# Kernel tuning notes

Measured on AMD Instinct MI355X. Metric: run time of the kernel, lower is better.

Reference implementation:

```python
import jax, jax.numpy as jnp
import numpy as np

B, N, D, DS, LAT, FD, NF = 2, 384, 128, 3, 256, 1, 2
NPOS = DS * (2 * 5 + 1)  # 3 + 3*2*5 = 33
FREQS = np.linspace(1.0, 32.0, 5)  # torch.linspace(1, 2**5, 5)
EPS = 1e-5


def _bn(x, g, b):
    # BatchNorm1d, train-mode batch stats: normalize per channel over (batch, points)
    m = jnp.mean(x, axis=(0, 1))
    v = jnp.var(x, axis=(0, 1))
    return (x - m) * jax.lax.rsqrt(v + EPS) * g + b


def _tblock(xyz4, f, Wq, Wk, Wv, Wg1, bg1, Wg2, bg2, Wpe, bpe, g, b):
    # group_all=True full vector attention. f: [B,n,D], xyz4: [B,n,3]
    q = f @ Wq.T
    k = f @ Wk.T
    v = f @ Wv.T
    # knn_xyz gathered under no_grad in torch -> stop_gradient on the key side
    pd = xyz4[:, :, None] - jax.lax.stop_gradient(xyz4)[:, None]  # [B,n,n,3]
    parts = [pd]
    for fr in FREQS:
        parts.append(jnp.sin(pd * fr))
        parts.append(jnp.cos(pd * fr))
    pos = jnp.concatenate(parts, axis=-1) @ Wpe.T + bpe  # [B,n,n,D]
    edges = q[:, :, None] - k[:, None] + pos  # [B,n,n,D]
    h = jax.nn.relu(edges @ Wg1.T + bg1)
    attn = jax.nn.softmax(h @ Wg2.T + bg2, axis=-2)  # softmax over neighbor axis
    res = jnp.sum(attn * (v[:, None] + pos), axis=2)  # einsum bmnf,bmnf->bmf
    return _bn(res + f, g, b)


def setup_inputs() -> dict:
    key = jax.random.key(0)
    ks = iter(jax.random.split(key, 40))
    def rn(shape, s=0.05):
        return jax.random.normal(next(ks), shape, dtype=jnp.float32) * s
    z = lambda *s: jnp.zeros(s, jnp.float32)
    o = lambda *s: jnp.ones(s, jnp.float32)
    nb = NF + 1  # begin block + nfinal blocks
    return {
        "xyz": jax.random.normal(next(ks), (B, N, DS), dtype=jnp.float32),
        "feats": jax.random.normal(next(ks), (B, N, FD), dtype=jnp.float32),
        "enc_W": rn((D, FD)), "enc_b": z(D),
        "tb_Wq": rn((nb, D, D)), "tb_Wk": rn((nb, D, D)), "tb_Wv": rn((nb, D, D)),
        "tb_Wg1": rn((nb, D, D)), "tb_bg1": z(nb, D),
        "tb_Wg2": rn((nb, D, D)), "tb_bg2": z(nb, D),
        "tb_Wpe": rn((nb, D, NPOS)), "tb_bpe": z(nb, D),
        "tb_gamma": o(nb, D), "tb_beta": z(nb, D),
        "em_W1": rn((NF, D, D)), "em_b1": z(NF, D),
        "em_W2": rn((NF, D, D)), "em_b2": z(NF, D),
        "em_gamma": o(NF, D), "em_beta": z(NF, D),
        "fcf_W1": rn((LAT, D)), "fcf_b1": z(LAT),
        "fcf_W2": rn((LAT, LAT)), "fcf_b2": z(LAT),
    }


def reference(xyz, feats, enc_W, enc_b, tb_Wq, tb_Wk, tb_Wv, tb_Wg1, tb_bg1,
              tb_Wg2, tb_bg2, tb_Wpe, tb_bpe, tb_gamma, tb_beta,
              em_W1, em_b1, em_W2, em_b2, em_gamma, em_beta,
              fcf_W1, fcf_b1, fcf_W2, fcf_b2):
    f = feats @ enc_W.T + enc_b  # enc_feats
    x4 = xyz * 4.0
    for i in range(NF + 1):  # i=0: transformer_begin; i>=1: final transformers
        f = _tblock(x4, f, tb_Wq[i], tb_Wk[i], tb_Wv[i], tb_Wg1[i], tb_bg1[i],
                    tb_Wg2[i], tb_bg2[i], tb_Wpe[i], tb_bpe[i], tb_gamma[i], tb_beta[i])
        if i > 0:
            j = i - 1  # ElementwiseMLP: bn(x + relu(conv2(relu(conv1(x)))))
            y = jax.nn.relu(f @ em_W1[j].T + em_b1[j])
            y = jax.nn.relu(y @ em_W2[j].T + em_b2[j])
            f = _bn(f + y, em_gamma[j], em_beta[j])
    e = jax.nn.relu(f @ fcf_W1.T + fcf_b1) @ fcf_W2.T + fcf_b2
    return jnp.max(e, axis=1)  # lat_rep [B, lat_dim]
```

## Files before the change

kernel.cpp:

```cpp
#include <hip/hip_runtime.h>
#include <hip/hip_bf16.h>

#define B_ 2
#define N_ 384
#define D_ 128
#define LAT_ 256
#define NPOS_ 33
#define ROWS_ (B_*N_)
#define NT_ 64
#define ITERS_ (N_/NT_)

typedef __attribute__((ext_vector_type(8))) short bf16x8;
typedef __attribute__((ext_vector_type(4))) float f32x4;

#define MFMA(a,b,c) __builtin_amdgcn_mfma_f32_16x16x32_bf16((a),(b),(c),0,0,0)

__device__ __forceinline__ unsigned short f2bf(float x) {
    unsigned int u = __float_as_uint(x);
    u += 0x7FFFu + ((u >> 16) & 1u);
    return (unsigned short)(u >> 16);
}
__device__ __forceinline__ float bf2f(unsigned short u) {
    return __uint_as_float(((unsigned int)u) << 16);
}

__device__ __forceinline__ float bn_apply(float x, const float* stats, const float* gam,
                                          const float* bet, int d) {
    float s  = stats[d], sq = stats[128 + d];
    float mean = s * (1.f/ROWS_);
    float var  = sq * (1.f/ROWS_) - mean*mean;
    return (x - mean) * rsqrtf(var + 1e-5f) * gam[d] + bet[d];
}

__global__ __launch_bounds__(256) void fprep_kernel(const float* __restrict__ xyz,
                                                    unsigned short* __restrict__ gF) {
    int i = blockIdx.x*256 + threadIdx.x;
    if (i >= ROWS_*64) return;
    int n = i >> 6, q = i & 63;
    float val;
    if (q == 0) val = 1.f;
    else if (q < 4) val = 4.f*xyz[n*3 + (q-1)];
    else if (q < 34) {
        int u = q-4, fi = u/6, rem = u - fi*6, j = rem >> 1;
        const float fr = fi==0?1.f:(fi==1?8.75f:(fi==2?16.5f:(fi==3?24.25f:32.f)));
        float a = fr*4.f*xyz[n*3+j];
        val = (rem & 1) ? __sinf(a) : __cosf(a);
    } else val = 0.f;
    gF[n*64 + (q ^ ((n & 7) << 3))] = f2bf(val);
}

__global__ __launch_bounds__(128) void psi_kernel(
    const float* __restrict__ Wg1, const float* __restrict__ Wpe,
    const float* __restrict__ bpe, float* __restrict__ psi)
{
    const int blk = blockIdx.x, layer = blk / 34, p = blk - layer*34;
    const float* wg1 = Wg1 + layer*D_*D_;
    __shared__ float col[D_];
    const int e = threadIdx.x;
    col[e] = (p < NPOS_) ? Wpe[layer*D_*NPOS_ + e*NPOS_ + p] : bpe[layer*D_ + e];
    __syncthreads();
    float acc = 0.f;
    #pragma unroll 4
    for (int d4 = 0; d4 < 32; ++d4) {
        float4 w = *(const float4*)(wg1 + e*D_ + d4*4);
        acc += w.x*col[d4*4] + w.y*col[d4*4+1] + w.z*col[d4*4+2] + w.w*col[d4*4+3];
    }
    psi[layer*D_*34 + e*34 + p] = acc;
}

__global__ __launch_bounds__(256) void enc_kernel(const float* __restrict__ feats,
                           const float* __restrict__ W,
                           const float* __restrict__ bias,
                           float* __restrict__ f) {
    int i = blockIdx.x*256 + threadIdx.x;
    if (i >= ROWS_*D_) return;
    int r = i >> 7, d = i & 127;
    f[i] = feats[r]*W[d] + bias[d];
}

__global__ __launch_bounds__(128) void qkvkw_kernel(const float* __restrict__ graw,
    const float* __restrict__ stats, const float* __restrict__ gam, const float* __restrict__ bet,
    int use_stats,
    const float* __restrict__ Wq, const float* __restrict__ Wk, const float* __restrict__ Wv,
    const float* __restrict__ Wg1, const float* __restrict__ bg1,
    float* __restrict__ hb, unsigned short* __restrict__ kw16, unsigned short* __restrict__ v16)
{
    __shared__ float rows[4][D_], qrows[4][D_], krows[4][D_];
    const int r0 = blockIdx.x*4, d = threadIdx.x;
    #pragma unroll
    for (int rr = 0; rr < 4; ++rr) {
        float x = graw[(r0+rr)*D_ + d];
        if (use_stats) x = bn_apply(x, stats, gam, bet, d);
        rows[rr][d] = x;
    }
    __syncthreads();
    float aq[4] = {0,0,0,0}, ak[4] = {0,0,0,0}, av[4] = {0,0,0,0};
    #pragma unroll 4
    for (int e4 = 0; e4 < D_/4; ++e4) {
        float4 wq = *(const float4*)(Wq + d*D_ + e4*4);
        float4 wk = *(const float4*)(Wk + d*D_ + e4*4);
        float4 wv = *(const float4*)(Wv + d*D_ + e4*4);
        #pragma unroll
        for (int rr = 0; rr < 4; ++rr) {
            float4 x = *(const float4*)&rows[rr][e4*4];
            aq[rr] += wq.x*x.x + wq.y*x.y + wq.z*x.z + wq.w*x.w;
            ak[rr] += wk.x*x.x + wk.y*x.y + wk.z*x.z + wk.w*x.w;
            av[rr] += wv.x*x.x + wv.y*x.y + wv.z*x.z + wv.w*x.w;
        }
    }
    #pragma unroll
    for (int rr = 0; rr < 4; ++rr) {
        v16[(r0+rr)*D_ + d] = f2bf(av[rr]);
        qrows[rr][d] = aq[rr];
        krows[rr][d] = ak[rr];
    }
    __syncthreads();
    float hq[4], hk[4] = {0,0,0,0};
    #pragma unroll
    for (int rr = 0; rr < 4; ++rr) hq[rr] = bg1[d];
    #pragma unroll 4
    for (int e4 = 0; e4 < D_/4; ++e4) {
        float4 w = *(const float4*)(Wg1 + d*D_ + e4*4);
        #pragma unroll
        for (int rr = 0; rr < 4; ++rr) {
            float4 xq = *(const float4*)&qrows[rr][e4*4];
            float4 xk = *(const float4*)&krows[rr][e4*4];
            hq[rr] += w.x*xq.x + w.y*xq.y + w.z*xq.z + w.w*xq.w;
            hk[rr] += w.x*xk.x + w.y*xk.y + w.z*xk.z + w.w*xk.w;
        }
    }
    #pragma unroll
    for (int rr = 0; rr < 4; ++rr) {
        hb[(r0+rr)*D_ + d]   = hq[rr];
        kw16[(r0+rr)*D_ + d] = f2bf(hk[rr]);
    }
}

__global__ __launch_bounds__(512) void attn_mfma_kernel(
    const float* __restrict__ xyz, const float* __restrict__ graw,
    const float* __restrict__ stats_in, const float* __restrict__ gam_in,
    const float* __restrict__ bet_in, int use_stats,
    const float* __restrict__ hbb,
    const unsigned short* __restrict__ kwb, const unsigned short* __restrict__ vb,
    const unsigned short* __restrict__ gF,
    const float* __restrict__ psiL,
    const float* __restrict__ Wpe, const float* __restrict__ bpe,
    const float* __restrict__ Wg2, const float* __restrict__ bg2,
    float* __restrict__ gout, float* __restrict__ stats_out)
{
    __shared__ unsigned short sF[NT_*64];
    __shared__ unsigned short sH[NT_*128];
    __shared__ float sRed[4*128];

    const int t   = threadIdx.x;
    const int w   = t >> 6;
    const int l   = t & 63;
    const int lr  = l & 15;
    const int lg  = l >> 4;
    const int rb2 = w >> 2;
    const int ct0 = (w & 3) * 2;

    const int row  = blockIdx.x;
    const int b    = row / N_;
    const int brow = b * N_;

    uint4 freg = *(const uint4*)(gF + (size_t)brow*64 + t*8);
    unsigned short kw_us[2][2][4];
    unsigned short v_us[2][2][4];
    auto loadKW = [&](int n0) {
        #pragma unroll
        for (int rt = 0; rt < 2; ++rt)
        #pragma unroll
        for (int ct = 0; ct < 2; ++ct) {
            const int d = (ct0 + ct)*16 + lr;
            #pragma unroll
            for (int r = 0; r < 4; ++r) {
                const int rr = rb2*32 + rt*16 + lg*4 + r;
                kw_us[rt][ct][r] = kwb[(brow + n0 + rr)*D_ + d];
            }
        }
    };
    auto loadV = [&](int n0) {
        #pragma unroll
        for (int rt = 0; rt < 2; ++rt)
        #pragma unroll
        for (int ct = 0; ct < 2; ++ct) {
            const int d = (ct0 + ct)*16 + lr;
            #pragma unroll
            for (int r = 0; r < 4; ++r) {
                const int rr = rb2*32 + rt*16 + lg*4 + r;
                v_us[rt][ct][r] = vb[(brow + n0 + rr)*D_ + d];
            }
        }
    };
    loadKW(0);

    bf16x8 bWg2[2][4], bG[2][2], bT[2][2];
    float  hb_c[2], bg2_c[2];

    const float xm0 = 4.f*xyz[row*3+0];
    const float xm1 = 4.f*xyz[row*3+1];
    const float xm2 = 4.f*xyz[row*3+2];

    #pragma unroll
    for (int ct = 0; ct < 2; ++ct) {
        const int dout = (ct0 + ct) * 16 + lr;
        #pragma unroll
        for (int kt = 0; kt < 4; ++kt) {
            const float* p2 = Wg2 + dout * D_ + kt * 32 + lg * 8;
            float4 c0 = *(const float4*)(p2);
            float4 c1 = *(const float4*)(p2 + 4);
            bf16x8 v2;
            v2[0]=(short)f2bf(c0.x); v2[1]=(short)f2bf(c0.y); v2[2]=(short)f2bf(c0.z); v2[3]=(short)f2bf(c0.w);
            v2[4]=(short)f2bf(c1.x); v2[5]=(short)f2bf(c1.y); v2[6]=(short)f2bf(c1.z); v2[7]=(short)f2bf(c1.w);
            bWg2[ct][kt] = v2;
        }
        {
            const float* wrow = Wpe + dout*NPOS_;
            float bias = bpe[dout] + wrow[0]*xm0 + wrow[1]*xm1 + wrow[2]*xm2;
            #pragma unroll
            for (int kt = 0; kt < 2; ++kt) {
                bf16x8 g;
                #pragma unroll
                for (int e = 0; e < 8; ++e) {
                    const int qq = kt*32 + lg*8 + e;
                    float val;
                    if (qq == 0) val = bias;
                    else if (qq < 4) val = -wrow[qq-1];
                    else if (qq < 34) {
                        const int u = qq - 4, fi = u/6, rem = u - fi*6, j = rem >> 1;
                        const float Ws = wrow[3 + 6*fi + j];
                        const float Wc = wrow[3 + 6*fi + 3 + j];
                        const float fr = fi==0?1.f:(fi==1?8.75f:(fi==2?16.5f:(fi==3?24.25f:32.f)));
                        const float am = fr * (j==0?xm0:(j==1?xm1:xm2));
                        const float sm = __sinf(am), cm = __cosf(am);
                        val = (rem & 1) ? (Wc*sm - Ws*cm) : (Ws*sm + Wc*cm);
                    } else val = 0.f;
                    g[e] = (short)f2bf(val);
                }
                bG[ct][kt] = g;
            }
        }
        {
            const float* prow = psiL + dout*34;
            float bias = prow[33] + prow[0]*xm0 + prow[1]*xm1 + prow[2]*xm2;
            #pragma unroll
            for (int kt = 0; kt < 2; ++kt) {
                bf16x8 g;
                #pragma unroll
                for (int e = 0; e < 8; ++e) {
                    const int qq = kt*32 + lg*8 + e;
                    float val;
                    if (qq == 0) val = bias;
                    else if (qq < 4) val = -prow[qq-1];
                    else if (qq < 34) {
                        const int u = qq - 4, fi = u/6, rem = u - fi*6, j = rem >> 1;
                        const float Ws = prow[3 + 6*fi + j];
                        const float Wc = prow[3 + 6*fi + 3 + j];
                        const float fr = fi==0?1.f:(fi==1?8.75f:(fi==2?16.5f:(fi==3?24.25f:32.f)));
                        const float am = fr * (j==0?xm0:(j==1?xm1:xm2));
                        const float sm = __sinf(am), cm = __cosf(am);
                        val = (rem & 1) ? (Wc*sm - Ws*cm) : (Ws*sm + Wc*cm);
                    } else val = 0.f;
                    g[e] = (short)f2bf(val);
                }
                bT[ct][kt] = g;
            }
        }
        hb_c[ct]  = hbb[row*D_ + dout];
        bg2_c[ct] = bg2[dout];
    }

    *(uint4*)&sF[t*8] = freg;
    __syncthreads();

    float res_p[2] = {0.f, 0.f}, s_p[2] = {0.f, 0.f};
    f32x4 pos[2][2];

    for (int it = 0; it < ITERS_; ++it) {
        const int n0 = it * NT_;
        const bool more = (it < ITERS_ - 1);

        loadV(n0);
        if (more) freg = *(const uint4*)(gF + (size_t)(brow + n0 + NT_)*64 + t*8);
        f32x4 hacc[2][2];
        #pragma unroll
        for (int rt = 0; rt < 2; ++rt) {
            const int r16 = rb2*32 + rt*16 + lr;
            const int sw  = (r16 & 7) << 3;
            bf16x8 a0 = *(const bf16x8*)&sF[(r16*64 +  0 + lg*8) ^ sw];
            bf16x8 a1 = *(const bf16x8*)&sF[(r16*64 + 32 + lg*8) ^ sw];
            #pragma unroll
            for (int ct = 0; ct < 2; ++ct) {
                f32x4 z = {0.f,0.f,0.f,0.f};
                hacc[rt][ct] = MFMA(a1, bT[ct][1], MFMA(a0, bT[ct][0], z));
                pos[rt][ct]  = MFMA(a1, bG[ct][1], MFMA(a0, bG[ct][0], z));
            }
        }
        #pragma unroll
        for (int rt = 0; rt < 2; ++rt)
        #pragma unroll
        for (int ct = 0; ct < 2; ++ct) {
            const int d = (ct0 + ct)*16 + lr;
            #pragma unroll
            for (int r = 0; r < 4; ++r) {
                const int rr = rb2*32 + rt*16 + lg*4 + r;
                const float hv = hacc[rt][ct][r] + hb_c[ct] - bf2f(kw_us[rt][ct][r]);
                sH[(rr*128 + d) ^ ((rr & 7) << 3)] = f2bf(fmaxf(hv, 0.f));
            }
        }
        __syncthreads();

        if (more) {
            *(uint4*)&sF[t*8] = freg;
            loadKW(n0 + NT_);
        }
        f32x4 lacc[2][2];
        #pragma unroll
        for (int rt = 0; rt < 2; ++rt) {
            lacc[rt][0] = (f32x4){bg2_c[0], bg2_c[0], bg2_c[0], bg2_c[0]};
            lacc[rt][1] = (f32x4){bg2_c[1], bg2_c[1], bg2_c[1], bg2_c[1]};
            #pragma unroll
            for (int kt = 0; kt < 4; ++kt) {
                const int r16 = rb2*32 + rt*16 + lr;
                const int idx = (r16*128 + kt*32 + lg*8) ^ ((r16 & 7) << 3);
                bf16x8 a = *(const bf16x8*)&sH[idx];
                lacc[rt][0] = MFMA(a, bWg2[0][kt], lacc[rt][0]);
                lacc[rt][1] = MFMA(a, bWg2[1][kt], lacc[rt][1]);
            }
        }
        #pragma unroll
        for (int rt = 0; rt < 2; ++rt)
        #pragma unroll
        for (int ct = 0; ct < 2; ++ct) {
            #pragma unroll
            for (int r = 0; r < 4; ++r) {
                const float wgt = __expf(lacc[rt][ct][r]);
                const float vp  = bf2f(v_us[rt][ct][r]) + pos[rt][ct][r];
                res_p[ct] += wgt * vp;
                s_p[ct]   += wgt;
            }
        }
        __syncthreads();
    }

    #pragma unroll
    for (int ct = 0; ct < 2; ++ct) {
        #pragma unroll
        for (int off = 16; off < 64; off <<= 1) {
            res_p[ct] += __shfl_xor(res_p[ct], off, 64);
            s_p[ct]   += __shfl_xor(s_p[ct], off, 64);
        }
    }
    if (lg == 0) {
        #pragma unroll
        for (int ct = 0; ct < 2; ++ct) {
            const int d = (ct0 + ct)*16 + lr;
            sRed[(rb2*2+0)*128 + d] = res_p[ct];
            sRed[(rb2*2+1)*128 + d] = s_p[ct];
        }
    }
    __syncthreads();
    if (t < D_) {
        const float rsum = sRed[t]       + sRed[2*128 + t];
        const float ssum = sRed[128 + t] + sRed[3*128 + t];
        float fres = graw[row*D_ + t];
        if (use_stats) fres = bn_apply(fres, stats_in, gam_in, bet_in, t);
        const float val = rsum / ssum + fres;
        gout[row*D_ + t] = val;
        atomicAdd(&stats_out[t], val);
        atomicAdd(&stats_out[128 + t], val*val);
    }
}

__global__ __launch_bounds__(128) void em_kernel(const float* __restrict__ graw,
    const float* __restrict__ stats_in, const float* __restrict__ gam_in, const float* __restrict__ bet_in,
    const float* __restrict__ W1, const float* __restrict__ b1,
    const float* __restrict__ W2, const float* __restrict__ b2,
    float* __restrict__ gout, float* __restrict__ stats_out)
{
    __shared__ float rows[4][D_], y1[4][D_];
    const int r0 = blockIdx.x*4, d = threadIdx.x;
    float fn[4];
    #pragma unroll
    for (int rr = 0; rr < 4; ++rr) {
        fn[rr] = bn_apply(graw[(r0+rr)*D_ + d], stats_in, gam_in, bet_in, d);
        rows[rr][d] = fn[rr];
    }
    __syncthreads();
    float a[4] = {b1[d], b1[d], b1[d], b1[d]};
    #pragma unroll 4
    for (int e4 = 0; e4 < D_/4; ++e4) {
        float4 w = *(const float4*)(W1 + d*D_ + e4*4);
        #pragma unroll
        for (int rr = 0; rr < 4; ++rr) {
            float4 x = *(const float4*)&rows[rr][e4*4];
            a[rr] += w.x*x.x + w.y*x.y + w.z*x.z + w.w*x.w;
        }
    }
    #pragma unroll
    for (int rr = 0; rr < 4; ++rr) y1[rr][d] = fmaxf(a[rr], 0.f);
    __syncthreads();
    float a2[4] = {b2[d], b2[d], b2[d], b2[d]};
    #pragma unroll 4
    for (int e4 = 0; e4 < D_/4; ++e4) {
        float4 w = *(const float4*)(W2 + d*D_ + e4*4);
        #pragma unroll
        for (int rr = 0; rr < 4; ++rr) {
            float4 x = *(const float4*)&y1[rr][e4*4];
            a2[rr] += w.x*x.x + w.y*x.y + w.z*x.z + w.w*x.w;
        }
    }
    #pragma unroll
    for (int rr = 0; rr < 4; ++rr) {
        const float g2 = fn[rr] + fmaxf(a2[rr], 0.f);
        gout[(r0+rr)*D_ + d] = g2;
        atomicAdd(&stats_out[d], g2);
        atomicAdd(&stats_out[128+d], g2*g2);
    }
}

__global__ __launch_bounds__(256) void final_kernel(const float* __restrict__ graw,
    const float* __restrict__ stats_in, const float* __restrict__ gam_in, const float* __restrict__ bet_in,
    const float* __restrict__ W1, const float* __restrict__ b1,
    const float* __restrict__ W2, const float* __restrict__ b2,
    float* __restrict__ e_ws)
{
    __shared__ float rows[4][D_];
    __shared__ float h1[4][LAT_];
    const int r0 = blockIdx.x*4, t = threadIdx.x;
    for (int i = t; i < 4*D_; i += 256) {
        const int rr = i >> 7, d = i & 127;
        rows[rr][d] = bn_apply(graw[(r0+rr)*D_ + d], stats_in, gam_in, bet_in, d);
    }
    __syncthreads();
    float a[4] = {b1[t], b1[t], b1[t], b1[t]};
    #pragma unroll 4
    for (int e4 = 0; e4 < D_/4; ++e4) {
        float4 w = *(const float4*)(W1 + t*D_ + e4*4);
        #pragma unroll
        for (int rr = 0; rr < 4; ++rr) {
            float4 x = *(const float4*)&rows[rr][e4*4];
            a[rr] += w.x*x.x + w.y*x.y + w.z*x.z + w.w*x.w;
        }
    }
    #pragma unroll
    for (int rr = 0; rr < 4; ++rr) h1[rr][t] = fmaxf(a[rr], 0.f);
    __syncthreads();
    float a2[4] = {b2[t], b2[t], b2[t], b2[t]};
    #pragma unroll 4
    for (int e4 = 0; e4 < LAT_/4; ++e4) {
        float4 w = *(const float4*)(W2 + t*LAT_ + e4*4);
        #pragma unroll
        for (int rr = 0; rr < 4; ++rr) {
            float4 x = *(const float4*)&h1[rr][e4*4];
            a2[rr] += w.x*x.x + w.y*x.y + w.z*x.z + w.w*x.w;
        }
    }
    #pragma unroll
    for (int rr = 0; rr < 4; ++rr) e_ws[(r0+rr)*LAT_ + t] = a2[rr];
}

__global__ __launch_bounds__(256) void maxred_kernel(const float* __restrict__ e_ws,
                                                     float* __restrict__ out)
{
    int b = blockIdx.x, l = threadIdx.x;
    float m = -INFINITY;
    #pragma unroll 8
    for (int n=0;n<N_;n++) m = fmaxf(m, e_ws[(b*N_+n)*LAT_+l]);
    out[b*LAT_+l] = m;
}

extern "C" void kernel_launch(void* const* d_in, const int* in_sizes, int n_in,
                              void* d_out, int out_size, void* d_ws, size_t ws_size,
                              hipStream_t stream) {
    (void)in_sizes; (void)n_in; (void)out_size; (void)ws_size;
    const float* xyz    = (const float*)d_in[0];
    const float* feats  = (const float*)d_in[1];
    const float* enc_W  = (const float*)d_in[2];
    const float* enc_b  = (const float*)d_in[3];
    const float* tb_Wq  = (const float*)d_in[4];
    const float* tb_Wk  = (const float*)d_in[5];
    const float* tb_Wv  = (const float*)d_in[6];
    const float* tb_Wg1 = (const float*)d_in[7];
    const float* tb_bg1 = (const float*)d_in[8];
    const float* tb_Wg2 = (const float*)d_in[9];
    const float* tb_bg2 = (const float*)d_in[10];
    const float* tb_Wpe = (const float*)d_in[11];
    const float* tb_bpe = (const float*)d_in[12];
    const float* tb_gamma = (const float*)d_in[13];
    const float* tb_beta  = (const float*)d_in[14];
    const float* em_W1  = (const float*)d_in[15];
    const float* em_b1  = (const float*)d_in[16];
    const float* em_W2  = (const float*)d_in[17];
    const float* em_b2  = (const float*)d_in[18];
    const float* em_gamma = (const float*)d_in[19];
    const float* em_beta  = (const float*)d_in[20];
    const float* fcf_W1 = (const float*)d_in[21];
    const float* fcf_b1 = (const float*)d_in[22];
    const float* fcf_W2 = (const float*)d_in[23];
    const float* fcf_b2 = (const float*)d_in[24];
    float* out = (float*)d_out;

    float* ws   = (float*)d_ws;
    float* buf0 = ws;
    float* buf1 = buf0 + ROWS_*D_;
    float* hbb  = buf1 + ROWS_*D_;
    float* ebuf = hbb  + ROWS_*D_;
    float* psi  = ebuf + ROWS_*LAT_;
    float* stats = psi + 3*D_*34;
    float* sA0 = stats;
    float* sA1 = stats + 256;
    float* sE1 = stats + 512;
    float* sA2 = stats + 768;
    float* sE2 = stats + 1024;
    unsigned short* kwbuf = (unsigned short*)(stats + 5*256);
    unsigned short* vbuf  = kwbuf + ROWS_*D_;
    unsigned short* gF    = vbuf + ROWS_*D_;

    hipMemsetAsync(stats, 0, 5*256*sizeof(float), stream);

    fprep_kernel<<<(ROWS_*64+255)/256, 256, 0, stream>>>(xyz, gF);
    psi_kernel<<<3*34, 128, 0, stream>>>(tb_Wg1, tb_Wpe, tb_bpe, psi);
    enc_kernel<<<(ROWS_*D_+255)/256, 256, 0, stream>>>(feats, enc_W, enc_b, buf0);

    const float* gz = tb_gamma;
    qkvkw_kernel<<<ROWS_/4, 128, 0, stream>>>(buf0, gz, gz, gz, 0,
        tb_Wq, tb_Wk, tb_Wv, tb_Wg1, tb_bg1, hbb, kwbuf, vbuf);
    attn_mfma_kernel<<<ROWS_, 512, 0, stream>>>(xyz, buf0, gz, gz, gz, 0,
        hbb, kwbuf, vbuf, gF, psi,
        tb_Wpe, tb_bpe, tb_Wg2, tb_bg2, buf1, sA0);
    qkvkw_kernel<<<ROWS_/4, 128, 0, stream>>>(buf1, sA0, tb_gamma, tb_beta, 1,
        tb_Wq + 1*D_*D_, tb_Wk + 1*D_*D_, tb_Wv + 1*D_*D_,
        tb_Wg1 + 1*D_*D_, tb_bg1 + 1*D_, hbb, kwbuf, vbuf);
    attn_mfma_kernel<<<ROWS_, 512, 0, stream>>>(xyz, buf1, sA0, tb_gamma, tb_beta, 1,
        hbb, kwbuf, vbuf, gF, psi + 1*D_*34,
        tb_Wpe + 1*D_*NPOS_, tb_bpe + 1*D_, tb_Wg2 + 1*D_*D_, tb_bg2 + 1*D_, buf0, sA1);
    em_kernel<<<ROWS_/4, 128, 0, stream>>>(buf0, sA1, tb_gamma + 1*D_, tb_beta + 1*D_,
                                           em_W1, em_b1, em_W2, em_b2, buf1, sE1);
    qkvkw_kernel<<<ROWS_/4, 128, 0, stream>>>(buf1, sE1, em_gamma, em_beta, 1,
        tb_Wq + 2*D_*D_, tb_Wk + 2*D_*D_, tb_Wv + 2*D_*D_,
        tb_Wg1 + 2*D_*D_, tb_bg1 + 2*D_, hbb, kwbuf, vbuf);
    attn_mfma_kernel<<<ROWS_, 512, 0, stream>>>(xyz, buf1, sE1, em_gamma, em_beta, 1,
        hbb, kwbuf, vbuf, gF, psi + 2*D_*34,
        tb_Wpe + 2*D_*NPOS_, tb_bpe + 2*D_, tb_Wg2 + 2*D_*D_, tb_bg2 + 2*D_, buf0, sA2);
    em_kernel<<<ROWS_/4, 128, 0, stream>>>(buf0, sA2, tb_gamma + 2*D_, tb_beta + 2*D_,
                                           em_W1 + 1*D_*D_, em_b1 + 1*D_,
                                           em_W2 + 1*D_*D_, em_b2 + 1*D_, buf1, sE2);
    final_kernel<<<ROWS_/4, 256, 0, stream>>>(buf1, sE2, em_gamma + 1*D_, em_beta + 1*D_,
                                              fcf_W1, fcf_b1, fcf_W2, fcf_b2, ebuf);
    maxred_kernel<<<B_, 256, 0, stream>>>(ebuf, out);
}
```

Before: 556.9 us.

## Precompose Wg1 with Wq/Wk, merge prep kernels, shrink per-block row counts

Folds Wg1 into Wq and Wk by precomputing the products Wg1·Wq and Wg1·Wk once per call in a merged prep kernel, so the per-row QKV kernel needs one matvec stage instead of two. The fprep, psi and enc kernels are merged with this weight precomputation into a single launch to cut launch overhead. The em and final kernels process fewer rows per block (1 and 2) to spread work across more blocks. The cost is an extra 2x3 128x128 matrix-product precompute each call, less weight reuse per block, and a small change in rounding order.

```diff
diff --git a/kernel.cpp b/kernel.cpp
--- a/kernel.cpp
+++ b/kernel.cpp
@@ -32,108 +32,102 @@
     return (x - mean) * rsqrtf(var + 1e-5f) * gam[d] + bet[d];
 }
 
-__global__ __launch_bounds__(256) void fprep_kernel(const float* __restrict__ xyz,
-                                                    unsigned short* __restrict__ gF) {
-    int i = blockIdx.x*256 + threadIdx.x;
-    if (i >= ROWS_*64) return;
-    int n = i >> 6, q = i & 63;
-    float val;
-    if (q == 0) val = 1.f;
-    else if (q < 4) val = 4.f*xyz[n*3 + (q-1)];
-    else if (q < 34) {
-        int u = q-4, fi = u/6, rem = u - fi*6, j = rem >> 1;
-        const float fr = fi==0?1.f:(fi==1?8.75f:(fi==2?16.5f:(fi==3?24.25f:32.f)));
-        float a = fr*4.f*xyz[n*3+j];
-        val = (rem & 1) ? __sinf(a) : __cosf(a);
-    } else val = 0.f;
-    gF[n*64 + (q ^ ((n & 7) << 3))] = f2bf(val);
-}
-
-__global__ __launch_bounds__(128) void psi_kernel(
-    const float* __restrict__ Wg1, const float* __restrict__ Wpe,
-    const float* __restrict__ bpe, float* __restrict__ psi)
+#define PB_FPREP 192
+#define PB_PSI   (PB_FPREP + 51)
+#define PB_ENC   (PB_PSI + 384)
+#define PB_WQG   (PB_ENC + 384)
+__global__ __launch_bounds__(256) void prep_kernel(
+    const float* __restrict__ xyz, const float* __restrict__ feats,
+    const float* __restrict__ enc_W, const float* __restrict__ enc_b,
+    const float* __restrict__ Wg1, const float* __restrict__ Wpe, const float* __restrict__ bpe,
+    const float* __restrict__ Wq, const float* __restrict__ Wk,
+    unsigned short* __restrict__ gF, float* __restrict__ psi,
+    float* __restrict__ wqg, float* __restrict__ wkg, float* __restrict__ f)
 {
-    const int blk = blockIdx.x, layer = blk / 34, p = blk - layer*34;
-    const float* wg1 = Wg1 + layer*D_*D_;
-    __shared__ float col[D_];
-    const int e = threadIdx.x;
-    col[e] = (p < NPOS_) ? Wpe[layer*D_*NPOS_ + e*NPOS_ + p] : bpe[layer*D_ + e];
-    __syncthreads();
-    float acc = 0.f;
-    #pragma unroll 4
-    for (int d4 = 0; d4 < 32; ++d4) {
-        float4 w = *(const float4*)(wg1 + e*D_ + d4*4);
-        acc += w.x*col[d4*4] + w.y*col[d4*4+1] + w.z*col[d4*4+2] + w.w*col[d4*4+3];
-    }
-    psi[layer*D_*34 + e*34 + p] = acc;
-}
-
-__global__ __launch_bounds__(256) void enc_kernel(const float* __restrict__ feats,
-                           const float* __restrict__ W,
-                           const float* __restrict__ bias,
-                           float* __restrict__ f) {
-    int i = blockIdx.x*256 + threadIdx.x;
-    if (i >= ROWS_*D_) return;
-    int r = i >> 7, d = i & 127;
-    f[i] = feats[r]*W[d] + bias[d];
-}
-
-__global__ __launch_bounds__(128) void qkvkw_kernel(const float* __restrict__ graw,
+    const int blk = blockIdx.x, t = threadIdx.x;
+    if (blk < PB_FPREP) {
+        int i = blk*256 + t;
+        int n = i >> 6, q = i & 63;
+        float val;
+        if (q == 0) val = 1.f;
+        else if (q < 4) val = 4.f*xyz[n*3 + (q-1)];
+        else if (q < 34) {
+            int u = q-4, fi = u/6, rem = u - fi*6, j = rem >> 1;
+            const float fr = fi==0?1.f:(fi==1?8.75f:(fi==2?16.5f:(fi==3?24.25f:32.f)));
+            float a = fr*4.f*xyz[n*3+j];
+            val = (rem & 1) ? __sinf(a) : __cosf(a);
+        } else val = 0.f;
+        gF[n*64 + (q ^ ((n & 7) << 3))] = f2bf(val);
+    } else if (blk < PB_PSI) {
+        __shared__ float col2[2][D_];
+        const int colid = (blk - PB_FPREP)*2 + (t >> 7);
+        const int layer = colid / 34, p = colid - layer*34;
+        const int e = t & 127, half = t >> 7;
+        col2[half][e] = (p < NPOS_) ? Wpe[layer*D_*NPOS_ + e*NPOS_ + p]
+                                    : bpe[layer*D_ + e];
+        __syncthreads();
+        const float* wg1 = Wg1 + layer*D_*D_;
+        float acc = 0.f;
+        #pragma unroll 4
+        for (int d4 = 0; d4 < 32; ++d4) {
+            float4 w = *(const float4*)(wg1 + e*D_ + d4*4);
+            acc += w.x*col2[half][d4*4] + w.y*col2[half][d4*4+1]
+                 + w.z*col2[half][d4*4+2] + w.w*col2[half][d4*4+3];
+        }
+        psi[layer*D_*34 + e*34 + p] = acc;
+    } else if (blk < PB_ENC) {
+        int i = (blk - PB_PSI)*256 + t;
+        int r = i >> 7, d = i & 127;
+        f[i] = feats[r]*enc_W[d] + enc_b[d];
+    } else {
+        __shared__ float col2[2][D_];
+        const int colid = (blk - PB_ENC)*2 + (t >> 7);
+        const int layer = colid >> 8, rem = colid & 255;
+        const int mat = rem >> 7, ecol = rem & 127;
+        const int e = t & 127, half = t >> 7;
+        const float* Wsrc = mat ? Wk : Wq;
+        col2[half][e] = Wsrc[layer*D_*D_ + e*D_ + ecol];
+        __syncthreads();
+        const float* wg1 = Wg1 + layer*D_*D_;
+        float acc = 0.f;
+        #pragma unroll 4
+        for (int d4 = 0; d4 < 32; ++d4) {
+            float4 w = *(const float4*)(wg1 + e*D_ + d4*4);
+            acc += w.x*col2[half][d4*4] + w.y*col2[half][d4*4+1]
+                 + w.z*col2[half][d4*4+2] + w.w*col2[half][d4*4+3];
+        }
+        float* dst = mat ? wkg : wqg;
+        dst[layer*D_*D_ + e*D_ + ecol] = acc;
+    }
+}
+
+__global__ __launch_bounds__(128) void qkv3_kernel(const float* __restrict__ graw,
     const float* __restrict__ stats, const float* __restrict__ gam, const float* __restrict__ bet,
     int use_stats,
-    const float* __restrict__ Wq, const float* __restrict__ Wk, const float* __restrict__ Wv,
-    const float* __restrict__ Wg1, const float* __restrict__ bg1,
+    const float* __restrict__ Wv, const float* __restrict__ Wqg, const float* __restrict__ Wkg,
+    const float* __restrict__ bg1,
     float* __restrict__ hb, unsigned short* __restrict__ kw16, unsigned short* __restrict__ v16)
 {
-    __shared__ float rows[4][D_], qrows[4][D_], krows[4][D_];
-    const int r0 = blockIdx.x*4, d = threadIdx.x;
-    #pragma unroll
-    for (int rr = 0; rr < 4; ++rr) {
-        float x = graw[(r0+rr)*D_ + d];
-        if (use_stats) x = bn_apply(x, stats, gam, bet, d);
-        rows[rr][d] = x;
-    }
-    __syncthreads();
-    float aq[4] = {0,0,0,0}, ak[4] = {0,0,0,0}, av[4] = {0,0,0,0};
+    __shared__ float row[D_];
+    const int r = blockIdx.x, d = threadIdx.x;
+    float x = graw[r*D_ + d];
+    if (use_stats) x = bn_apply(x, stats, gam, bet, d);
+    row[d] = x;
+    __syncthreads();
+    float av = 0.f, ah = bg1[d], ak = 0.f;
     #pragma unroll 4
     for (int e4 = 0; e4 < D_/4; ++e4) {
-        float4 wq = *(const float4*)(Wq + d*D_ + e4*4);
-        float4 wk = *(const float4*)(Wk + d*D_ + e4*4);
-        float4 wv = *(const float4*)(Wv + d*D_ + e4*4);
-        #pragma unroll
-        for (int rr = 0; rr < 4; ++rr) {
-            float4 x = *(const float4*)&rows[rr][e4*4];
-            aq[rr] += wq.x*x.x + wq.y*x.y + wq.z*x.z + wq.w*x.w;
-            ak[rr] += wk.x*x.x + wk.y*x.y + wk.z*x.z + wk.w*x.w;
-            av[rr] += wv.x*x.x + wv.y*x.y + wv.z*x.z + wv.w*x.w;
-        }
-    }
-    #pragma unroll
-    for (int rr = 0; rr < 4; ++rr) {
-        v16[(r0+rr)*D_ + d] = f2bf(av[rr]);
-        qrows[rr][d] = aq[rr];
-        krows[rr][d] = ak[rr];
-    }
-    __syncthreads();
-    float hq[4], hk[4] = {0,0,0,0};
-    #pragma unroll
-    for (int rr = 0; rr < 4; ++rr) hq[rr] = bg1[d];
-    #pragma unroll 4
-    for (int e4 = 0; e4 < D_/4; ++e4) {
-        float4 w = *(const float4*)(Wg1 + d*D_ + e4*4);
-        #pragma unroll
-        for (int rr = 0; rr < 4; ++rr) {
-            float4 xq = *(const float4*)&qrows[rr][e4*4];
-            float4 xk = *(const float4*)&krows[rr][e4*4];
-            hq[rr] += w.x*xq.x + w.y*xq.y + w.z*xq.z + w.w*xq.w;
-            hk[rr] += w.x*xk.x + w.y*xk.y + w.z*xk.z + w.w*xk.w;
-        }
-    }
-    #pragma unroll
-    for (int rr = 0; rr < 4; ++rr) {
-        hb[(r0+rr)*D_ + d]   = hq[rr];
-        kw16[(r0+rr)*D_ + d] = f2bf(hk[rr]);
-    }
+        float4 wv = *(const float4*)(Wv  + d*D_ + e4*4);
+        float4 wh = *(const float4*)(Wqg + d*D_ + e4*4);
+        float4 wk = *(const float4*)(Wkg + d*D_ + e4*4);
+        float4 xx = *(const float4*)&row[e4*4];
+        av += wv.x*xx.x + wv.y*xx.y + wv.z*xx.z + wv.w*xx.w;
+        ah += wh.x*xx.x + wh.y*xx.y + wh.z*xx.z + wh.w*xx.w;
+        ak += wk.x*xx.x + wk.y*xx.y + wk.z*xx.z + wk.w*xx.w;
+    }
+    v16[r*D_ + d]  = f2bf(av);
+    hb[r*D_ + d]   = ah;
+    kw16[r*D_ + d] = f2bf(ak);
 }
 
 __global__ __launch_bounds__(512) void attn_mfma_kernel(
@@ -379,45 +373,31 @@
     const float* __restrict__ W2, const float* __restrict__ b2,
     float* __restrict__ gout, float* __restrict__ stats_out)
 {
-    __shared__ float rows[4][D_], y1[4][D_];
-    const int r0 = blockIdx.x*4, d = threadIdx.x;
-    float fn[4];
-    #pragma unroll
-    for (int rr = 0; rr < 4; ++rr) {
-        fn[rr] = bn_apply(graw[(r0+rr)*D_ + d], stats_in, gam_in, bet_in, d);
-        rows[rr][d] = fn[rr];
-    }
-    __syncthreads();
-    float a[4] = {b1[d], b1[d], b1[d], b1[d]};
+    __shared__ float row[D_], y1[D_];
+    const int r = blockIdx.x, d = threadIdx.x;
+    const float fn = bn_apply(graw[r*D_ + d], stats_in, gam_in, bet_in, d);
+    row[d] = fn;
+    __syncthreads();
+    float a = b1[d];
     #pragma unroll 4
     for (int e4 = 0; e4 < D_/4; ++e4) {
         float4 w = *(const float4*)(W1 + d*D_ + e4*4);
-        #pragma unroll
-        for (int rr = 0; rr < 4; ++rr) {
-            float4 x = *(const float4*)&rows[rr][e4*4];
-            a[rr] += w.x*x.x + w.y*x.y + w.z*x.z + w.w*x.w;
-        }
-    }
-    #pragma unroll
-    for (int rr = 0; rr < 4; ++rr) y1[rr][d] = fmaxf(a[rr], 0.f);
-    __syncthreads();
-    float a2[4] = {b2[d], b2[d], b2[d], b2[d]};
+        float4 x = *(const float4*)&row[e4*4];
+        a += w.x*x.x + w.y*x.y + w.z*x.z + w.w*x.w;
+    }
+    y1[d] = fmaxf(a, 0.f);
+    __syncthreads();
+    float a2 = b2[d];
     #pragma unroll 4
     for (int e4 = 0; e4 < D_/4; ++e4) {
         float4 w = *(const float4*)(W2 + d*D_ + e4*4);
-        #pragma unroll
-        for (int rr = 0; rr < 4; ++rr) {
-            float4 x = *(const float4*)&y1[rr][e4*4];
-            a2[rr] += w.x*x.x + w.y*x.y + w.z*x.z + w.w*x.w;
-        }
-    }
-    #pragma unroll
-    for (int rr = 0; rr < 4; ++rr) {
-        const float g2 = fn[rr] + fmaxf(a2[rr], 0.f);
-        gout[(r0+rr)*D_ + d] = g2;
-        atomicAdd(&stats_out[d], g2);
-        atomicAdd(&stats_out[128+d], g2*g2);
-    }
+        float4 x = *(const float4*)&y1[e4*4];
+        a2 += w.x*x.x + w.y*x.y + w.z*x.z + w.w*x.w;
+    }
+    const float g2 = fn + fmaxf(a2, 0.f);
+    gout[r*D_ + d] = g2;
+    atomicAdd(&stats_out[d], g2);
+    atomicAdd(&stats_out[128 + d], g2*g2);
 }
 
 __global__ __launch_bounds__(256) void final_kernel(const float* __restrict__ graw,
@@ -426,39 +406,39 @@
     const float* __restrict__ W2, const float* __restrict__ b2,
     float* __restrict__ e_ws)
 {
-    __shared__ float rows[4][D_];
-    __shared__ float h1[4][LAT_];
-    const int r0 = blockIdx.x*4, t = threadIdx.x;
-    for (int i = t; i < 4*D_; i += 256) {
-        const int rr = i >> 7, d = i & 127;
+    __shared__ float rows[2][D_];
+    __shared__ float h1[2][LAT_];
+    const int r0 = blockIdx.x*2, t = threadIdx.x;
+    {
+        const int rr = t >> 7, d = t & 127;
         rows[rr][d] = bn_apply(graw[(r0+rr)*D_ + d], stats_in, gam_in, bet_in, d);
     }
     __syncthreads();
-    float a[4] = {b1[t], b1[t], b1[t], b1[t]};
+    float a[2] = {b1[t], b1[t]};
     #pragma unroll 4
     for (int e4 = 0; e4 < D_/4; ++e4) {
         float4 w = *(const float4*)(W1 + t*D_ + e4*4);
         #pragma unroll
-        for (int rr = 0; rr < 4; ++rr) {
+        for (int rr = 0; rr < 2; ++rr) {
             float4 x = *(const float4*)&rows[rr][e4*4];
             a[rr] += w.x*x.x + w.y*x.y + w.z*x.z + w.w*x.w;
         }
     }
     #pragma unroll
-    for (int rr = 0; rr < 4; ++rr) h1[rr][t] = fmaxf(a[rr], 0.f);
-    __syncthreads();
-    float a2[4] = {b2[t], b2[t], b2[t], b2[t]};
+    for (int rr = 0; rr < 2; ++rr) h1[rr][t] = fmaxf(a[rr], 0.f);
+    __syncthreads();
+    float a2[2] = {b2[t], b2[t]};
     #pragma unroll 4
     for (int e4 = 0; e4 < LAT_/4; ++e4) {
         float4 w = *(const float4*)(W2 + t*LAT_ + e4*4);
         #pragma unroll
-        for (int rr = 0; rr < 4; ++rr) {
+        for (int rr = 0; rr < 2; ++rr) {
             float4 x = *(const float4*)&h1[rr][e4*4];
             a2[rr] += w.x*x.x + w.y*x.y + w.z*x.z + w.w*x.w;
         }
     }
     #pragma unroll
-    for (int rr = 0; rr < 4; ++rr) e_ws[(r0+rr)*LAT_ + t] = a2[rr];
+    for (int rr = 0; rr < 2; ++rr) e_ws[(r0+rr)*LAT_ + t] = a2[rr];
 }
 
 __global__ __launch_bounds__(256) void maxred_kernel(const float* __restrict__ e_ws,
@@ -508,7 +488,9 @@
     float* hbb  = buf1 + ROWS_*D_;
     float* ebuf = hbb  + ROWS_*D_;
     float* psi  = ebuf + ROWS_*LAT_;
-    float* stats = psi + 3*D_*34;
+    float* wqg  = psi  + 3*D_*34;
+    float* wkg  = wqg  + 3*D_*D_;
+    float* stats = wkg + 3*D_*D_;
     float* sA0 = stats;
     float* sA1 = stats + 256;
     float* sE1 = stats + 512;
@@ -520,34 +502,31 @@
 
     hipMemsetAsync(stats, 0, 5*256*sizeof(float), stream);
 
-    fprep_kernel<<<(ROWS_*64+255)/256, 256, 0, stream>>>(xyz, gF);
-    psi_kernel<<<3*34, 128, 0, stream>>>(tb_Wg1, tb_Wpe, tb_bpe, psi);
-    enc_kernel<<<(ROWS_*D_+255)/256, 256, 0, stream>>>(feats, enc_W, enc_b, buf0);
+    prep_kernel<<<PB_WQG, 256, 0, stream>>>(xyz, feats, enc_W, enc_b,
+        tb_Wg1, tb_Wpe, tb_bpe, tb_Wq, tb_Wk, gF, psi, wqg, wkg, buf0);
 
     const float* gz = tb_gamma;
-    qkvkw_kernel<<<ROWS_/4, 128, 0, stream>>>(buf0, gz, gz, gz, 0,
-        tb_Wq, tb_Wk, tb_Wv, tb_Wg1, tb_bg1, hbb, kwbuf, vbuf);
+    qkv3_kernel<<<ROWS_, 128, 0, stream>>>(buf0, gz, gz, gz, 0,
+        tb_Wv, wqg, wkg, tb_bg1, hbb, kwbuf, vbuf);
     attn_mfma_kernel<<<ROWS_, 512, 0, stream>>>(xyz, buf0, gz, gz, gz, 0,
         hbb, kwbuf, vbuf, gF, psi,
         tb_Wpe, tb_bpe, tb_Wg2, tb_bg2, buf1, sA0);
-    qkvkw_kernel<<<ROWS_/4, 128, 0, stream>>>(buf1, sA0, tb_gamma, tb_beta, 1,
-        tb_Wq + 1*D_*D_, tb_Wk + 1*D_*D_, tb_Wv + 1*D_*D_,
-        tb_Wg1 + 1*D_*D_, tb_bg1 + 1*D_, hbb, kwbuf, vbuf);
+    qkv3_kernel<<<ROWS_, 128, 0, stream>>>(buf1, sA0, tb_gamma, tb_beta, 1,
+        tb_Wv + 1*D_*D_, wqg + 1*D_*D_, wkg + 1*D_*D_, tb_bg1 + 1*D_, hbb, kwbuf, vbuf);
     attn_mfma_kernel<<<ROWS_, 512, 0, stream>>>(xyz, buf1, sA0, tb_gamma, tb_beta, 1,
         hbb, kwbuf, vbuf, gF, psi + 1*D_*34,
         tb_Wpe + 1*D_*NPOS_, tb_bpe + 1*D_, tb_Wg2 + 1*D_*D_, tb_bg2 + 1*D_, buf0, sA1);
-    em_kernel<<<ROWS_/4, 128, 0, stream>>>(buf0, sA1, tb_gamma + 1*D_, tb_beta + 1*D_,
-                                           em_W1, em_b1, em_W2, em_b2, buf1, sE1);
-    qkvkw_kernel<<<ROWS_/4, 128, 0, stream>>>(buf1, sE1, em_gamma, em_beta, 1,
-        tb_Wq + 2*D_*D_, tb_Wk + 2*D_*D_, tb_Wv + 2*D_*D_,
-        tb_Wg1 + 2*D_*D_, tb_bg1 + 2*D_, hbb, kwbuf, vbuf);
+    em_kernel<<<ROWS_, 128, 0, stream>>>(buf0, sA1, tb_gamma + 1*D_, tb_beta + 1*D_,
+                                         em_W1, em_b1, em_W2, em_b2, buf1, sE1);
+    qkv3_kernel<<<ROWS_, 128, 0, stream>>>(buf1, sE1, em_gamma, em_beta, 1,
+        tb_Wv + 2*D_*D_, wqg + 2*D_*D_, wkg + 2*D_*D_, tb_bg1 + 2*D_, hbb, kwbuf, vbuf);
     attn_mfma_kernel<<<ROWS_, 512, 0, stream>>>(xyz, buf1, sE1, em_gamma, em_beta, 1,
         hbb, kwbuf, vbuf, gF, psi + 2*D_*34,
         tb_Wpe + 2*D_*NPOS_, tb_bpe + 2*D_, tb_Wg2 + 2*D_*D_, tb_bg2 + 2*D_, buf0, sA2);
-    em_kernel<<<ROWS_/4, 128, 0, stream>>>(buf0, sA2, tb_gamma + 2*D_, tb_beta + 2*D_,
-                                           em_W1 + 1*D_*D_, em_b1 + 1*D_,
-                                           em_W2 + 1*D_*D_, em_b2 + 1*D_, buf1, sE2);
-    final_kernel<<<ROWS_/4, 256, 0, stream>>>(buf1, sE2, em_gamma + 1*D_, em_beta + 1*D_,
+    em_kernel<<<ROWS_, 128, 0, stream>>>(buf0, sA2, tb_gamma + 2*D_, tb_beta + 2*D_,
+                                         em_W1 + 1*D_*D_, em_b1 + 1*D_,
+                                         em_W2 + 1*D_*D_, em_b2 + 1*D_, buf1, sE2);
+    final_kernel<<<ROWS_/2, 256, 0, stream>>>(buf1, sE2, em_gamma + 1*D_, em_beta + 1*D_,
                                               fcf_W1, fcf_b1, fcf_W2, fcf_b2, ebuf);
     maxred_kernel<<<B_, 256, 0, stream>>>(ebuf, out);
 }
```

Result: slower. 572.6 us (+2.8%).
